# Kernel tuning notes

Measured on AMD Instinct MI355X. Metric: run time of the kernel, lower is better.

## Reference

```python
import jax, jax.numpy as jnp
import numpy as np

B, W, DIN, DOUT, H = 256, 20, 1024, 1024, 1280
EPS = 1e-5
SLOPE = 0.01  # torch LeakyReLU default negative_slope


def setup_inputs() -> dict:
    key = jax.random.key(0)
    ks = jax.random.split(key, 16)
    s = lambda fan_in: 1.0 / np.sqrt(fan_in)
    return {
        'embs': jax.random.normal(ks[0], (B, W, DIN), jnp.float32),
        'W1': jax.random.uniform(ks[1], (W, DIN, H), jnp.float32, -s(DIN), s(DIN)),
        'b1': jax.random.uniform(ks[2], (W, H), jnp.float32, -s(DIN), s(DIN)),
        'g1': jnp.ones((W, H), jnp.float32), 'bn1': jnp.zeros((W, H), jnp.float32),
        'W2': jax.random.uniform(ks[3], (W, H, H), jnp.float32, -s(H), s(H)),
        'b2': jax.random.uniform(ks[4], (W, H), jnp.float32, -s(H), s(H)),
        'g2': jnp.ones((W, H), jnp.float32), 'bn2': jnp.zeros((W, H), jnp.float32),
        'W3': jax.random.uniform(ks[5], (W, H, H), jnp.float32, -s(H), s(H)),
        'b3': jax.random.uniform(ks[6], (W, H), jnp.float32, -s(H), s(H)),
        'g3': jnp.ones((W, H), jnp.float32), 'bn3': jnp.zeros((W, H), jnp.float32),
        'W4': jax.random.uniform(ks[7], (W, H, DOUT), jnp.float32, -s(H), s(H)),
        'b4': jax.random.uniform(ks[8], (W, DOUT), jnp.float32, -s(H), s(H)),
    }


def _layernorm(x, g, b):
    # x: [B, W, H]; g, b: [W, H] (per-word affine params)
    mu = jnp.mean(x, axis=-1, keepdims=True)
    var = jnp.mean(jnp.square(x - mu), axis=-1, keepdims=True)
    return (x - mu) * jax.lax.rsqrt(var + EPS) * g + b


def _leaky_relu(x):
    return jnp.where(x >= 0, x, SLOPE * x)


def reference(embs, W1, b1, g1, bn1, W2, b2, g2, bn2, W3, b3, g3, bn3, W4, b4):
    # Stacked per-word towers: equivalent to the torch per-word Python loop.
    # embs: [B, W, DIN] -> out: [B, W, DOUT]
    h = jnp.einsum('bwi,wih->bwh', embs, W1) + b1
    h = _leaky_relu(_layernorm(h, g1, bn1))
    h = jnp.einsum('bwh,whk->bwk', h, W2) + b2
    h = _leaky_relu(_layernorm(h, g2, bn2))
    h = jnp.einsum('bwh,whk->bwk', h, W3) + b3
    h = _leaky_relu(_layernorm(h, g3, bn3))
    out = jnp.einsum('bwh,who->bwo', h, W4) + b4
    return out
```

## Files before the change

### kernel.cpp

```cpp
#include <hip/hip_runtime.h>
#include <hip/hip_bf16.h>


typedef unsigned short u16;
typedef __attribute__((ext_vector_type(8))) short bf16x8;
typedef __attribute__((ext_vector_type(4))) float f32x4;

constexpr int CB = 256;
constexpr int CW = 20;
constexpr int CDIN = 1024;
constexpr int CDOUT = 1024;
constexpr int CH = 1280;
constexpr float CEPS = 1e-5f;
constexpr float CSLOPE = 0.01f;

__device__ __forceinline__ u16 f2bf(float f) {
    union { float f; unsigned u; } v; v.f = f;
    unsigned r = v.u + 0x7fffu + ((v.u >> 16) & 1u);
    return (u16)(r >> 16);
}
__device__ __forceinline__ unsigned pk2(float a, float b) {
    return (unsigned)f2bf(a) | ((unsigned)f2bf(b) << 16);
}

template <int K, int N>
__global__ __launch_bounds__(256, 2) void gemm_kernel(
    const u16* __restrict__ Ab, const float* __restrict__ Bw,
    const float* __restrict__ bias, float* __restrict__ Out)
{
    constexpr int NB = N / 128;
    constexpr int NK = K / 32;
    __shared__ u16 As[2][128 * 40];
    __shared__ u16 Bs[2][128 * 40];

    const int t   = threadIdx.x;
    const int bid = blockIdx.x;
    const int mb  = bid & 1;
    const int nb  = (bid >> 1) % NB;
    const int w   = bid / (2 * NB);

    const int m0g = mb * 128;
    const int n0g = nb * 128;

    const int lane = t & 63;
    const int wid  = t >> 6;
    const int m0 = (wid >> 1) * 64;
    const int n0 = (wid & 1) * 64;
    const int lrow = lane & 15;
    const int kg   = lane >> 4;

    const int ar  = t >> 1;
    const int akq = (t & 1) << 4;
    const u16* agp = Ab + ((size_t)(m0g + ar) * CW + w) * K + akq;

    const int bn = t & 127;
    const int bh = t >> 7;
    const float* bgp = Bw + (size_t)w * K * N + (size_t)bh * 16 * N + (n0g + bn);

    f32x4 acc[4][4];
    #pragma unroll
    for (int i = 0; i < 4; ++i)
        #pragma unroll
        for (int j = 0; j < 4; ++j)
            acc[i][j] = (f32x4){0.f, 0.f, 0.f, 0.f};

    uint4 a0, a1;
    float bstg[16];

    auto loadA = [&](int k0) {
        const uint4* p = reinterpret_cast<const uint4*>(agp + k0);
        a0 = p[0]; a1 = p[1];
    };
    auto loadB = [&](int k0) {
        const float* p = bgp + (size_t)k0 * N;
        #pragma unroll
        for (int i = 0; i < 16; ++i) bstg[i] = p[(size_t)i * N];
    };
    auto writeA = [&](int buf) {
        *reinterpret_cast<uint4*>(&As[buf][ar * 40 + akq])     = a0;
        *reinterpret_cast<uint4*>(&As[buf][ar * 40 + akq + 8]) = a1;
    };
    auto writeB = [&](int buf) {
        uint4 p0, p1;
        p0.x = pk2(bstg[0],  bstg[1]);  p0.y = pk2(bstg[2],  bstg[3]);
        p0.z = pk2(bstg[4],  bstg[5]);  p0.w = pk2(bstg[6],  bstg[7]);
        p1.x = pk2(bstg[8],  bstg[9]);  p1.y = pk2(bstg[10], bstg[11]);
        p1.z = pk2(bstg[12], bstg[13]); p1.w = pk2(bstg[14], bstg[15]);
        *reinterpret_cast<uint4*>(&Bs[buf][bn * 40 + bh * 16])     = p0;
        *reinterpret_cast<uint4*>(&Bs[buf][bn * 40 + bh * 16 + 8]) = p1;
    };
    auto compute = [&](int buf) {
        bf16x8 af[4], bfr[4];
        #pragma unroll
        for (int i = 0; i < 4; ++i)
            af[i] = *reinterpret_cast<const bf16x8*>(
                &As[buf][(m0 + i * 16 + lrow) * 40 + kg * 8]);
        #pragma unroll
        for (int j = 0; j < 4; ++j)
            bfr[j] = *reinterpret_cast<const bf16x8*>(
                &Bs[buf][(n0 + j * 16 + lrow) * 40 + kg * 8]);
        #pragma unroll
        for (int i = 0; i < 4; ++i)
            #pragma unroll
            for (int j = 0; j < 4; ++j)
                acc[i][j] = __builtin_amdgcn_mfma_f32_16x16x32_bf16(
                    af[i], bfr[j], acc[i][j], 0, 0, 0);
    };

    loadA(0); loadB(0);
    writeA(0); writeB(0);
    __syncthreads();

    int buf = 0;
    for (int ks = 0; ks < NK; ++ks) {
        if (ks + 1 < NK) { loadA((ks + 1) * 32); loadB((ks + 1) * 32); }
        compute(buf);
        if (ks + 1 < NK) { writeA(buf ^ 1); writeB(buf ^ 1); }
        __syncthreads();
        buf ^= 1;
    }

    const int rb = (lane >> 4) * 4;
    #pragma unroll
    for (int j = 0; j < 4; ++j) {
        const int gn = n0g + n0 + j * 16 + lrow;
        const float bv = bias[(size_t)w * N + gn];
        #pragma unroll
        for (int i = 0; i < 4; ++i) {
            const int gm = m0g + m0 + i * 16 + rb;
            #pragma unroll
            for (int r = 0; r < 4; ++r) {
                Out[((size_t)(gm + r) * CW + w) * N + gn] = acc[i][j][r] + bv;
            }
        }
    }
}

__global__ __launch_bounds__(320) void ln_lrelu_kernel(
    const float* __restrict__ h, const float* __restrict__ g,
    const float* __restrict__ bta, u16* __restrict__ out)
{
    const int row = blockIdx.x;
    const int w = row % CW;
    const int t = threadIdx.x;

    const float4 v = reinterpret_cast<const float4*>(h + (size_t)row * CH)[t];
    float s  = v.x + v.y + v.z + v.w;
    float sq = v.x * v.x + v.y * v.y + v.z * v.z + v.w * v.w;
    #pragma unroll
    for (int o = 32; o > 0; o >>= 1) {
        s  += __shfl_down(s, o, 64);
        sq += __shfl_down(sq, o, 64);
    }
    __shared__ float ss[5], sg[5];
    const int lane = t & 63, wv = t >> 6;
    if (lane == 0) { ss[wv] = s; sg[wv] = sq; }
    __syncthreads();
    float S = 0.f, Q = 0.f;
    #pragma unroll
    for (int i = 0; i < 5; ++i) { S += ss[i]; Q += sg[i]; }
    const float mean = S * (1.0f / CH);
    const float var  = Q * (1.0f / CH) - mean * mean;
    const float rstd = rsqrtf(var + CEPS);

    const float4 gg = reinterpret_cast<const float4*>(g   + (size_t)w * CH)[t];
    const float4 bb = reinterpret_cast<const float4*>(bta + (size_t)w * CH)[t];
    float4 y;
    y.x = (v.x - mean) * rstd * gg.x + bb.x;
    y.y = (v.y - mean) * rstd * gg.y + bb.y;
    y.z = (v.z - mean) * rstd * gg.z + bb.z;
    y.w = (v.w - mean) * rstd * gg.w + bb.w;
    y.x = y.x >= 0.f ? y.x : CSLOPE * y.x;
    y.y = y.y >= 0.f ? y.y : CSLOPE * y.y;
    y.z = y.z >= 0.f ? y.z : CSLOPE * y.z;
    y.w = y.w >= 0.f ? y.w : CSLOPE * y.w;
    ushort4 o4;
    o4.x = f2bf(y.x); o4.y = f2bf(y.y); o4.z = f2bf(y.z); o4.w = f2bf(y.w);
    reinterpret_cast<ushort4*>(out + (size_t)row * CH)[t] = o4;
}

__global__ void cvt_kernel(const float* __restrict__ in, u16* __restrict__ out,
                           int n4)
{
    const int i = blockIdx.x * blockDim.x + threadIdx.x;
    if (i < n4) {
        const float4 v = reinterpret_cast<const float4*>(in)[i];
        ushort4 o;
        o.x = f2bf(v.x); o.y = f2bf(v.y); o.z = f2bf(v.z); o.w = f2bf(v.w);
        reinterpret_cast<ushort4*>(out)[i] = o;
    }
}

extern "C" void kernel_launch(void* const* d_in, const int* in_sizes, int n_in,
                              void* d_out, int out_size, void* d_ws, size_t ws_size,
                              hipStream_t stream)
{
    const float* embs = (const float*)d_in[0];
    const float* W1  = (const float*)d_in[1];
    const float* b1  = (const float*)d_in[2];
    const float* g1  = (const float*)d_in[3];
    const float* bn1 = (const float*)d_in[4];
    const float* W2  = (const float*)d_in[5];
    const float* b2  = (const float*)d_in[6];
    const float* g2  = (const float*)d_in[7];
    const float* bn2 = (const float*)d_in[8];
    const float* W3  = (const float*)d_in[9];
    const float* b3  = (const float*)d_in[10];
    const float* g3  = (const float*)d_in[11];
    const float* bn3 = (const float*)d_in[12];
    const float* W4  = (const float*)d_in[13];
    const float* b4  = (const float*)d_in[14];

    char* ws = (char*)d_ws;
    float* h_raw = (float*)ws;
    u16*   a_bf  = (u16*)(ws + 26214400);
    u16*   e_bf  = (u16*)(ws + 26214400 + 13107200);

    const int n4 = CB * CW * CDIN / 4;
    cvt_kernel<<<n4 / 256, 256, 0, stream>>>(embs, e_bf, n4);

    gemm_kernel<CDIN, CH><<<CW * 2 * (CH / 128), 256, 0, stream>>>(e_bf, W1, b1, h_raw);
    ln_lrelu_kernel<<<CB * CW, 320, 0, stream>>>(h_raw, g1, bn1, a_bf);
    gemm_kernel<CH, CH><<<CW * 2 * (CH / 128), 256, 0, stream>>>(a_bf, W2, b2, h_raw);
    ln_lrelu_kernel<<<CB * CW, 320, 0, stream>>>(h_raw, g2, bn2, a_bf);
    gemm_kernel<CH, CH><<<CW * 2 * (CH / 128), 256, 0, stream>>>(a_bf, W3, b3, h_raw);
    ln_lrelu_kernel<<<CB * CW, 320, 0, stream>>>(h_raw, g3, bn3, a_bf);
    gemm_kernel<CH, CDOUT><<<CW * 2 * (CDOUT / 128), 256, 0, stream>>>(a_bf, W4, b4, (float*)d_out);
}
```

Before: 329.7 us.

## Shrink GEMM tiles to 64x64, swizzle blocks across XCDs, fuse input bf16 conversion

The GEMM tile shrinks from 128x128 to 64x64, with 2x2 MFMA tiles per wave and launch bounds raised to 6 blocks per CU, so the grid has four times as many workgroups to fill the GPU. Block IDs are remapped so consecutive logical tiles land on the same XCD, which is meant to improve L2 reuse of weights. The first layer now reads fp32 embeddings and converts them to bf16 inside the GEMM, removing the separate conversion kernel and its round trip through memory. The cost is less data reuse per tile, so each weight and activation element is fetched more times.

```diff
diff --git a/kernel.cpp b/kernel.cpp
--- a/kernel.cpp
+++ b/kernel.cpp
@@ -23,86 +23,99 @@
     return (unsigned)f2bf(a) | ((unsigned)f2bf(b) << 16);
 }
 
-template <int K, int N>
-__global__ __launch_bounds__(256, 2) void gemm_kernel(
-    const u16* __restrict__ Ab, const float* __restrict__ Bw,
+template <int K, int N, bool AF32>
+__global__ __launch_bounds__(256, 6) void gemm_kernel(
+    const void* __restrict__ Aptr, const float* __restrict__ Bw,
     const float* __restrict__ bias, float* __restrict__ Out)
 {
-    constexpr int NB = N / 128;
-    constexpr int NK = K / 32;
-    __shared__ u16 As[2][128 * 40];
-    __shared__ u16 Bs[2][128 * 40];
+    constexpr int NB  = N / 64;
+    constexpr int NK  = K / 32;
+    constexpr int NWG = 4 * NB * CW;
+    constexpr int CPX = NWG / 8;
+
+    __shared__ u16 As[2][64 * 40];
+    __shared__ u16 Bs[2][64 * 40];
 
     const int t   = threadIdx.x;
     const int bid = blockIdx.x;
-    const int mb  = bid & 1;
-    const int nb  = (bid >> 1) % NB;
-    const int w   = bid / (2 * NB);
-
-    const int m0g = mb * 128;
-    const int n0g = nb * 128;
+    const int logical = (bid & 7) * CPX + (bid >> 3);
+    const int mb = logical & 3;
+    const int nb = (logical >> 2) % NB;
+    const int w  = logical / (4 * NB);
+
+    const int m0g = mb * 64;
+    const int n0g = nb * 64;
 
     const int lane = t & 63;
     const int wid  = t >> 6;
-    const int m0 = (wid >> 1) * 64;
-    const int n0 = (wid & 1) * 64;
+    const int m0 = (wid >> 1) * 32;
+    const int n0 = (wid & 1) * 32;
     const int lrow = lane & 15;
     const int kg   = lane >> 4;
 
-    const int ar  = t >> 1;
-    const int akq = (t & 1) << 4;
-    const u16* agp = Ab + ((size_t)(m0g + ar) * CW + w) * K + akq;
-
-    const int bn = t & 127;
-    const int bh = t >> 7;
-    const float* bgp = Bw + (size_t)w * K * N + (size_t)bh * 16 * N + (n0g + bn);
-
-    f32x4 acc[4][4];
-    #pragma unroll
-    for (int i = 0; i < 4; ++i)
-        #pragma unroll
-        for (int j = 0; j < 4; ++j)
+    const int ar = t >> 2;
+    const int ac = (t & 3) * 8;
+    const u16*   agp  = (const u16*)Aptr   + ((size_t)(m0g + ar) * CW + w) * K + ac;
+    const float* agpf = (const float*)Aptr + ((size_t)(m0g + ar) * CW + w) * K + ac;
+
+    const int bn = t & 63;
+    const int bq = t >> 6;
+    const float* bgp = Bw + (size_t)w * K * N + (size_t)bq * 8 * N + (n0g + bn);
+
+    f32x4 acc[2][2];
+    #pragma unroll
+    for (int i = 0; i < 2; ++i)
+        #pragma unroll
+        for (int j = 0; j < 2; ++j)
             acc[i][j] = (f32x4){0.f, 0.f, 0.f, 0.f};
 
-    uint4 a0, a1;
-    float bstg[16];
+    uint4 a0;
+    float4 af0, af1;
+    float bstg[8];
 
     auto loadA = [&](int k0) {
-        const uint4* p = reinterpret_cast<const uint4*>(agp + k0);
-        a0 = p[0]; a1 = p[1];
+        if constexpr (AF32) {
+            const float4* p = reinterpret_cast<const float4*>(agpf + k0);
+            af0 = p[0]; af1 = p[1];
+        } else {
+            a0 = *reinterpret_cast<const uint4*>(agp + k0);
+        }
     };
     auto loadB = [&](int k0) {
         const float* p = bgp + (size_t)k0 * N;
         #pragma unroll
-        for (int i = 0; i < 16; ++i) bstg[i] = p[(size_t)i * N];
+        for (int i = 0; i < 8; ++i) bstg[i] = p[(size_t)i * N];
     };
     auto writeA = [&](int buf) {
-        *reinterpret_cast<uint4*>(&As[buf][ar * 40 + akq])     = a0;
-        *reinterpret_cast<uint4*>(&As[buf][ar * 40 + akq + 8]) = a1;
+        if constexpr (AF32) {
+            uint4 pk;
+            pk.x = pk2(af0.x, af0.y); pk.y = pk2(af0.z, af0.w);
+            pk.z = pk2(af1.x, af1.y); pk.w = pk2(af1.z, af1.w);
+            *reinterpret_cast<uint4*>(&As[buf][ar * 40 + ac]) = pk;
+        } else {
+            *reinterpret_cast<uint4*>(&As[buf][ar * 40 + ac]) = a0;
+        }
     };
     auto writeB = [&](int buf) {
-        uint4 p0, p1;
-        p0.x = pk2(bstg[0],  bstg[1]);  p0.y = pk2(bstg[2],  bstg[3]);
-        p0.z = pk2(bstg[4],  bstg[5]);  p0.w = pk2(bstg[6],  bstg[7]);
-        p1.x = pk2(bstg[8],  bstg[9]);  p1.y = pk2(bstg[10], bstg[11]);
-        p1.z = pk2(bstg[12], bstg[13]); p1.w = pk2(bstg[14], bstg[15]);
-        *reinterpret_cast<uint4*>(&Bs[buf][bn * 40 + bh * 16])     = p0;
-        *reinterpret_cast<uint4*>(&Bs[buf][bn * 40 + bh * 16 + 8]) = p1;
+        uint4 pk;
+        pk.x = pk2(bstg[0], bstg[1]); pk.y = pk2(bstg[2], bstg[3]);
+        pk.z = pk2(bstg[4], bstg[5]); pk.w = pk2(bstg[6], bstg[7]);
+        *reinterpret_cast<uint4*>(&Bs[buf][bn * 40 + bq * 8]) = pk;
     };
     auto compute = [&](int buf) {
-        bf16x8 af[4], bfr[4];
-        #pragma unroll
-        for (int i = 0; i < 4; ++i)
+        bf16x8 af[2], bfr[2];
+        #pragma unroll
+        for (int i = 0; i < 2; ++i)
             af[i] = *reinterpret_cast<const bf16x8*>(
                 &As[buf][(m0 + i * 16 + lrow) * 40 + kg * 8]);
         #pragma unroll
-        for (int j = 0; j < 4; ++j)
+        for (int j = 0; j < 2; ++j)
             bfr[j] = *reinterpret_cast<const bf16x8*>(
                 &Bs[buf][(n0 + j * 16 + lrow) * 40 + kg * 8]);
         #pragma unroll
-        for (int i = 0; i < 4; ++i)
+        for (int i = 0; i < 2; ++i)
             #pragma unroll
-            for (int j = 0; j < 4; ++j)
+            for (int j = 0; j < 2; ++j)
                 acc[i][j] = __builtin_amdgcn_mfma_f32_16x16x32_bf16(
                     af[i], bfr[j], acc[i][j], 0, 0, 0);
     };
@@ -122,11 +135,11 @@
 
     const int rb = (lane >> 4) * 4;
     #pragma unroll
-    for (int j = 0; j < 4; ++j) {
+    for (int j = 0; j < 2; ++j) {
         const int gn = n0g + n0 + j * 16 + lrow;
         const float bv = bias[(size_t)w * N + gn];
         #pragma unroll
-        for (int i = 0; i < 4; ++i) {
+        for (int i = 0; i < 2; ++i) {
             const int gm = m0g + m0 + i * 16 + rb;
             #pragma unroll
             for (int r = 0; r < 4; ++r) {
@@ -177,18 +190,6 @@
     ushort4 o4;
     o4.x = f2bf(y.x); o4.y = f2bf(y.y); o4.z = f2bf(y.z); o4.w = f2bf(y.w);
     reinterpret_cast<ushort4*>(out + (size_t)row * CH)[t] = o4;
-}
-
-__global__ void cvt_kernel(const float* __restrict__ in, u16* __restrict__ out,
-                           int n4)
-{
-    const int i = blockIdx.x * blockDim.x + threadIdx.x;
-    if (i < n4) {
-        const float4 v = reinterpret_cast<const float4*>(in)[i];
-        ushort4 o;
-        o.x = f2bf(v.x); o.y = f2bf(v.y); o.z = f2bf(v.z); o.w = f2bf(v.w);
-        reinterpret_cast<ushort4*>(out)[i] = o;
-    }
 }
 
 extern "C" void kernel_launch(void* const* d_in, const int* in_sizes, int n_in,
@@ -214,16 +215,12 @@
     char* ws = (char*)d_ws;
     float* h_raw = (float*)ws;
     u16*   a_bf  = (u16*)(ws + 26214400);
-    u16*   e_bf  = (u16*)(ws + 26214400 + 13107200);
-
-    const int n4 = CB * CW * CDIN / 4;
-    cvt_kernel<<<n4 / 256, 256, 0, stream>>>(embs, e_bf, n4);
-
-    gemm_kernel<CDIN, CH><<<CW * 2 * (CH / 128), 256, 0, stream>>>(e_bf, W1, b1, h_raw);
+
+    gemm_kernel<CDIN, CH, true><<<4 * (CH / 64) * CW, 256, 0, stream>>>(embs, W1, b1, h_raw);
     ln_lrelu_kernel<<<CB * CW, 320, 0, stream>>>(h_raw, g1, bn1, a_bf);
-    gemm_kernel<CH, CH><<<CW * 2 * (CH / 128), 256, 0, stream>>>(a_bf, W2, b2, h_raw);
+    gemm_kernel<CH, CH, false><<<4 * (CH / 64) * CW, 256, 0, stream>>>(a_bf, W2, b2, h_raw);
     ln_lrelu_kernel<<<CB * CW, 320, 0, stream>>>(h_raw, g2, bn2, a_bf);
-    gemm_kernel<CH, CH><<<CW * 2 * (CH / 128), 256, 0, stream>>>(a_bf, W3, b3, h_raw);
+    gemm_kernel<CH, CH, false><<<4 * (CH / 64) * CW, 256, 0, stream>>>(a_bf, W3, b3, h_raw);
     ln_lrelu_kernel<<<CB * CW, 320, 0, stream>>>(h_raw, g3, bn3, a_bf);
-    gemm_kernel<CH, CDOUT><<<CW * 2 * (CDOUT / 128), 256, 0, stream>>>(a_bf, W4, b4, (float*)d_out);
-}
+    gemm_kernel<CH, CDOUT, false><<<4 * (CDOUT / 64) * CW, 256, 0, stream>>>(a_bf, W4, b4, (float*)d_out);
+}
```

Result: no change. 334.9 us (+1.6%).
